# Performance work log

Hardware: AMD Instinct MI355X
Metric: run time of the kernel (lower is better)

The kernel has to match this reference:

```python
import jax, jax.numpy as jnp
import numpy as np

B, S, D = 2, 2048, 2048
NH, NKV, HD = 16, 4, 128
REP = NH // NKV
EPS = 1e-6
ROPE_THETA = 1e6


def setup_inputs() -> dict:
    key = jax.random.key(0)
    ks = jax.random.split(key, 6)
    x = jax.random.normal(ks[0], (B, S, D), jnp.float32)
    # real rotary embeddings: [S, HD]
    inv_freq = 1.0 / (ROPE_THETA ** (np.arange(0, HD, 2, dtype=np.float64) / HD))
    freqs = np.outer(np.arange(S, dtype=np.float64), inv_freq)
    emb = np.concatenate([freqs, freqs], axis=-1)
    cos = jnp.asarray(np.cos(emb), jnp.float32)
    sin = jnp.asarray(np.sin(emb), jnp.float32)
    scale = 1.0 / np.sqrt(D)
    Wq = jax.random.normal(ks[1], (D, NH * HD), jnp.float32) * scale   # [in, out]
    Wk = jax.random.normal(ks[2], (D, NKV * HD), jnp.float32) * scale
    Wv = jax.random.normal(ks[3], (D, NKV * HD), jnp.float32) * scale
    Wo = jax.random.normal(ks[4], (NH * HD, D), jnp.float32) * (1.0 / np.sqrt(NH * HD))
    q_norm_w = jnp.ones((HD,), jnp.float32)
    k_norm_w = jnp.ones((HD,), jnp.float32)
    return dict(x=x, cos=cos, sin=sin, Wq=Wq, Wk=Wk, Wv=Wv, Wo=Wo,
                q_norm_w=q_norm_w, k_norm_w=k_norm_w)


def _rms_norm(h, w):
    var = jnp.mean(h * h, axis=-1, keepdims=True)
    return w * (h * jax.lax.rsqrt(var + EPS))


def _rotate_half(h):
    h1, h2 = jnp.split(h, 2, axis=-1)
    return jnp.concatenate([-h2, h1], axis=-1)


def reference(x, cos, sin, Wq, Wk, Wv, Wo, q_norm_w, k_norm_w):
    b, s, _ = x.shape
    q = (x @ Wq).reshape(b, s, NH, HD)
    k = (x @ Wk).reshape(b, s, NKV, HD)
    v = (x @ Wv).reshape(b, s, NKV, HD)
    # per-head QK RMSNorm
    q = _rms_norm(q, q_norm_w)
    k = _rms_norm(k, k_norm_w)
    # RoPE: cos/sin [S,HD] -> broadcast over batch and heads
    c = cos[None, :, None, :]
    s_ = sin[None, :, None, :]
    q = q * c + _rotate_half(q) * s_
    k = k * c + _rotate_half(k) * s_
    # GQA: group q heads per kv head instead of materializing repeat_kv
    qg = q.reshape(b, s, NKV, REP, HD)
    scores = jnp.einsum('bqgrd,bkgd->bgrqk', qg, k) / np.sqrt(HD)
    causal = jnp.tril(jnp.ones((s, s), bool))  # [q,k]
    scores = jnp.where(causal, scores, -jnp.inf)
    probs = jax.nn.softmax(scores.astype(jnp.float32), axis=-1).astype(q.dtype)
    out = jnp.einsum('bgrqk,bkgd->bqgrd', probs, v).reshape(b, s, NH * HD)
    return out @ Wo
```

## Files before the change

### kernel.cpp

```cpp
#include <hip/hip_runtime.h>
#include <hip/hip_bf16.h>
#include <math.h>

#define B_ 2
#define S_ 2048
#define D_ 2048
#define NH_ 16
#define NKV_ 4
#define HD_ 128
#define EPS_ 1e-6f
#define SCALE_ 0.08838834764831845f
#define LOG2E_ 1.4426950408889634f
#define KOFF_ 2048
#define VOFF_ 2560
#define MINIT_ -1e30f

typedef float f32x4 __attribute__((ext_vector_type(4)));
typedef short bf16x8 __attribute__((ext_vector_type(8)));
typedef short short4v __attribute__((ext_vector_type(4)));
typedef float float4v __attribute__((ext_vector_type(4)));
typedef unsigned uint2v __attribute__((ext_vector_type(2)));
typedef unsigned uint4v __attribute__((ext_vector_type(4)));

static __device__ __forceinline__ short f2bf(float f) {
    union { float f; unsigned u; } x{f};
    unsigned r = (x.u + 0x7fff + ((x.u >> 16) & 1)) >> 16;
    return (short)r;
}
static __device__ __forceinline__ float bf2f(short s) {
    union { unsigned u; float f; } x; x.u = ((unsigned)(unsigned short)s) << 16; return x.f;
}
static __device__ __forceinline__ unsigned pack_bf2(float a, float b) {
    return __builtin_amdgcn_perm(__builtin_bit_cast(unsigned, b),
                                 __builtin_bit_cast(unsigned, a), 0x07060302u);
}

#define AS1(p) ((const __attribute__((address_space(1))) void*)(p))
#define AS3(p) ((__attribute__((address_space(3))) void*)(p))
static __device__ __forceinline__ void async16(const void* g, void* l) {
    __builtin_amdgcn_global_load_lds(AS1(g), AS3(l), 16, 0, 0);
}
#define SB_() __builtin_amdgcn_sched_barrier(0)

__global__ __launch_bounds__(256) void cast_kernel(const float* __restrict__ in,
                                                   short* __restrict__ out) {
    size_t i = ((size_t)blockIdx.x * 256 + threadIdx.x) * 4;
    float4v v = *(const float4v*)(in + i);
    short4v o; o.x = f2bf(v.x); o.y = f2bf(v.y); o.z = f2bf(v.z); o.w = f2bf(v.w);
    *(short4v*)(out + i) = o;
}

__global__ __launch_bounds__(256) void transpose_all_kernel(const float* __restrict__ Wq,
                                                            const float* __restrict__ Wk,
                                                            const float* __restrict__ Wv,
                                                            const float* __restrict__ Wo,
                                                            short* __restrict__ Wt,
                                                            short* __restrict__ Wot) {
    __shared__ float tile[64][65];
    const int bx = blockIdx.x, by = blockIdx.y;
    const float* src; short* dst; int N, nb;
    if (bx < 32)      { src = Wq; dst = Wt;                         N = 2048; nb = bx; }
    else if (bx < 40) { src = Wk; dst = Wt + (size_t)KOFF_ * 2048;  N = 512;  nb = bx - 32; }
    else if (bx < 48) { src = Wv; dst = Wt + (size_t)VOFF_ * 2048;  N = 512;  nb = bx - 40; }
    else              { src = Wo; dst = Wot;                        N = 2048; nb = bx - 48; }
    const int n0 = nb * 64, k0 = by * 64;
    const int tid = threadIdx.x;
    for (int r = 0; r < 16; ++r) {
        int k = r * 4 + (tid >> 6);
        int n = tid & 63;
        tile[k][n] = src[(size_t)(k0 + k) * N + n0 + n];
    }
    __syncthreads();
    for (int r = 0; r < 4; ++r) {
        int n  = r * 16 + (tid >> 4);
        int kk = (tid & 15) * 4;
        short4v o4;
        o4.x = f2bf(tile[kk + 0][n]); o4.y = f2bf(tile[kk + 1][n]);
        o4.z = f2bf(tile[kk + 2][n]); o4.w = f2bf(tile[kk + 3][n]);
        *(short4v*)&dst[(size_t)(n0 + n) * 2048 + k0 + kk] = o4;
    }
}

__global__ __launch_bounds__(512, 2) void gemm_oproj_kernel(const short* __restrict__ A,
                                                            const short* __restrict__ Bt,
                                                            float* __restrict__ C) {
    __shared__ __align__(16) short smem[49152];
    short* A0 = smem;
    short* A1 = smem + 8192;
    short* B0 = smem + 16384;
    short* B1 = smem + 32768;

    const int tid  = threadIdx.x;
    const int orig = blockIdx.y * 8 + blockIdx.x;
    const int swz  = (orig & 7) * 32 + (orig >> 3);
    const int bn = swz & 7, bm = swz >> 3;
    const int wave = tid >> 6, lane = tid & 63;
    const int quad = lane >> 4, l16 = lane & 15;
    const int wr = wave >> 2, wc = wave & 3;

    const short* Ag = A  + (size_t)(bm * 128) * 2048;
    const short* Bg = Bt + (size_t)(bn * 256) * 2048;

    f32x4 acc[4][4];
#pragma unroll
    for (int i = 0; i < 4; ++i)
#pragma unroll
        for (int j = 0; j < 4; ++j) acc[i][j] = (f32x4){0.f, 0.f, 0.f, 0.f};

    bf16x8 a[4][2], b0[2][2], b1[2][2];

    auto stage_half = [&](const short* gpanel, int t, int h, short* lslot) {
#pragma unroll
        for (int u = 0; u < 2; ++u) {
            int ci = u * 512 + tid;
            int r  = ci >> 3;
            int cb = ((ci & 7) * 16) ^ ((r & 7) << 4);
            async16(gpanel + (size_t)(h * 128 + r) * 2048 + t * 64 + (cb >> 1),
                    lslot + h * 8192 + ci * 8);
        }
    };

#define OLDA_(lbuf) \
    _Pragma("unroll") for (int mt = 0; mt < 4; ++mt) \
    _Pragma("unroll") for (int ks = 0; ks < 2; ++ks) { \
        int row_ = wr * 64 + mt * 16 + l16; \
        int cb_  = (ks * 64 + quad * 16) ^ ((row_ & 7) << 4); \
        a[mt][ks] = *(const bf16x8*)&(lbuf)[row_ * 64 + (cb_ >> 1)]; \
    }
#define OLDB_(lbuf, qn, breg) \
    _Pragma("unroll") for (int ntl = 0; ntl < 2; ++ntl) \
    _Pragma("unroll") for (int ks = 0; ks < 2; ++ks) { \
        int row_ = wc * 64 + (qn) * 32 + ntl * 16 + l16; \
        int cb_  = (ks * 64 + quad * 16) ^ ((row_ & 7) << 4); \
        breg[ntl][ks] = *(const bf16x8*)&(lbuf)[row_ * 64 + (cb_ >> 1)]; \
    }
#define OBAR_() __builtin_amdgcn_s_barrier()
#define OMFMA_(qn, breg) do { \
    __builtin_amdgcn_s_setprio(1); \
    _Pragma("unroll") for (int mt = 0; mt < 4; ++mt) \
    _Pragma("unroll") for (int ntl = 0; ntl < 2; ++ntl) \
    _Pragma("unroll") for (int ks = 0; ks < 2; ++ks) \
        acc[mt][(qn) * 2 + ntl] = __builtin_amdgcn_mfma_f32_16x16x32_bf16( \
            a[mt][ks], breg[ntl][ks], acc[mt][(qn) * 2 + ntl], 0, 0, 0); \
    __builtin_amdgcn_s_setprio(0); __builtin_amdgcn_s_barrier(); } while (0)

    stage_half(Bg, 0, 0, B0); stage_half(Bg, 0, 1, B0);
    stage_half(Ag, 0, 0, A0);
    asm volatile("s_waitcnt vmcnt(0)" ::: "memory");
    __builtin_amdgcn_s_barrier();

#pragma unroll 1
    for (int i = 0; i < 16; ++i) {
        const int tE = 2 * i, tO = 2 * i + 1;
        const bool more = (i < 15);

        stage_half(Ag, tO, 0, A1);
        stage_half(Bg, tO, 0, B1); stage_half(Bg, tO, 1, B1);
        OLDA_(A0); OLDB_(B0, 0, b0);
        OBAR_();
        OMFMA_(0, b0);

        if (more) {
            stage_half(Ag, tE + 2, 0, A0);
            asm volatile("s_waitcnt vmcnt(2)" ::: "memory");
        } else {
            asm volatile("s_waitcnt vmcnt(0)" ::: "memory");
        }
        OLDB_(B0, 1, b1);
        OBAR_();
        OMFMA_(1, b1);

        if (more) { stage_half(Bg, tE + 2, 0, B0); stage_half(Bg, tE + 2, 1, B0); }
        OLDA_(A1); OLDB_(B1, 0, b0);
        OBAR_();
        OMFMA_(0, b0);

        if (more) { asm volatile("s_waitcnt vmcnt(0)" ::: "memory"); }
        OLDB_(B1, 1, b1);
        OBAR_();
        OMFMA_(1, b1);
    }

#pragma unroll
    for (int mt = 0; mt < 4; ++mt)
#pragma unroll
        for (int nt = 0; nt < 4; ++nt)
#pragma unroll
            for (int j = 0; j < 4; ++j) {
                int row = bm * 128 + wr * 64 + mt * 16 + quad * 4 + j;
                int col = bn * 256 + wc * 64 + nt * 16 + l16;
                C[(size_t)row * 2048 + col] = acc[mt][nt][j];
            }
#undef OLDA_
#undef OLDB_
#undef OBAR_
#undef OMFMA_
}

#define QKV_ITERS 16

__global__ __launch_bounds__(512, 2) void qkv_fused_kernel(const short* __restrict__ xb,
                                                           const short* __restrict__ Wt,
                                                           const float* __restrict__ cosb,
                                                           const float* __restrict__ sinb,
                                                           const float* __restrict__ qw,
                                                           const float* __restrict__ kw,
                                                           short* __restrict__ q_rope,
                                                           short* __restrict__ k_rope,
                                                           short* __restrict__ vtr) {
    __shared__ __align__(16) short smem[65536];

    short* A0 = smem;
    short* A1 = smem + 8192;
    short* B0 = smem + 16384;
    short* B1 = smem + 40960;

    const int tid  = threadIdx.x;
    const int orig = blockIdx.y * 8 + blockIdx.x;
    const int swz  = (orig & 7) * 32 + (orig >> 3);
    const int bn = swz >> 5, bm = swz & 31;
    const int wave = tid >> 6, lane = tid & 63;
    const int quad = lane >> 4, l16 = lane & 15;
    const int wr = wave >> 2, wc = wave & 3;

    const short* Ag = xb + (size_t)(bm * 128) * 2048;
    const short* Bg = Wt + (size_t)(bn * 384) * 2048;

    f32x4 acc[4][6];
#pragma unroll
    for (int i = 0; i < 4; ++i)
#pragma unroll
        for (int j = 0; j < 6; ++j) acc[i][j] = (f32x4){0.f, 0.f, 0.f, 0.f};

    bf16x8 a[4][2], b0[3][2], b1[3][2];

    auto stage_half = [&](const short* gpanel, int t, int h, short* lslot) {
#pragma unroll
        for (int u = 0; u < 2; ++u) {
            int ci = u * 512 + tid;
            int r  = ci >> 3;
            int cb = ((ci & 7) * 16) ^ ((r & 7) << 4);
            async16(gpanel + (size_t)(h * 128 + r) * 2048 + t * 64 + (cb >> 1),
                    lslot + h * 8192 + ci * 8);
        }
    };

#define LDA_(lbuf) \
    _Pragma("unroll") for (int mt = 0; mt < 4; ++mt) \
    _Pragma("unroll") for (int ks = 0; ks < 2; ++ks) { \
        int row_ = wr * 64 + mt * 16 + l16; \
        int cb_  = (ks * 64 + quad * 16) ^ ((row_ & 7) << 4); \
        a[mt][ks] = *(const bf16x8*)&(lbuf)[row_ * 64 + (cb_ >> 1)]; \
    }
#define LDB_(lbuf, qn, breg) \
    _Pragma("unroll") for (int ntl = 0; ntl < 3; ++ntl) \
    _Pragma("unroll") for (int ks = 0; ks < 2; ++ks) { \
        int row_ = wc * 96 + (qn) * 48 + ntl * 16 + l16; \
        int cb_  = (ks * 64 + quad * 16) ^ ((row_ & 7) << 4); \
        breg[ntl][ks] = *(const bf16x8*)&(lbuf)[row_ * 64 + (cb_ >> 1)]; \
    }
#define PH_BAR() do { __builtin_amdgcn_sched_barrier(0); __builtin_amdgcn_s_barrier(); } while (0)
#define PH_MFMA24(qn, breg) do { \
        __builtin_amdgcn_s_setprio(1); \
        _Pragma("unroll") for (int mt = 0; mt < 4; ++mt) \
        _Pragma("unroll") for (int ntl = 0; ntl < 3; ++ntl) \
        _Pragma("unroll") for (int ks = 0; ks < 2; ++ks) \
            acc[mt][(qn) * 3 + ntl] = __builtin_amdgcn_mfma_f32_16x16x32_bf16( \
                a[mt][ks], breg[ntl][ks], acc[mt][(qn) * 3 + ntl], 0, 0, 0); \
        __builtin_amdgcn_s_setprio(0); \
        __builtin_amdgcn_sched_barrier(0); __builtin_amdgcn_s_barrier(); } while (0)

    stage_half(Bg, 0, 0, B0); stage_half(Bg, 0, 1, B0); stage_half(Bg, 0, 2, B0);
    stage_half(Ag, 0, 0, A0);
    stage_half(Ag, 1, 0, A1);
    asm volatile("s_waitcnt vmcnt(2)" ::: "memory");
    __builtin_amdgcn_s_barrier();

#pragma unroll 1
    for (int i = 0; i < QKV_ITERS; ++i) {
        const int tE = 2 * i, tO = 2 * i + 1;
        const bool more = (i < QKV_ITERS - 1);

        LDA_(A0); LDB_(B0, 0, b0);
        stage_half(Bg, tO, 0, B1); stage_half(Bg, tO, 1, B1); stage_half(Bg, tO, 2, B1);
        PH_BAR();
        PH_MFMA24(0, b0);

        LDB_(B0, 1, b1);
        if (more) {
            stage_half(Ag, tE + 2, 0, A0);
            asm volatile("s_waitcnt vmcnt(2)" ::: "memory");
        } else {
            asm volatile("s_waitcnt vmcnt(0)" ::: "memory");
        }
        PH_BAR();
        PH_MFMA24(1, b1);

        LDA_(A1); LDB_(B1, 0, b0);
        if (more) { stage_half(Bg, tE + 2, 0, B0); stage_half(Bg, tE + 2, 1, B0); stage_half(Bg, tE + 2, 2, B0); }
        PH_BAR();
        PH_MFMA24(0, b0);

        LDB_(B1, 1, b1);
        if (more) {
            stage_half(Ag, tO + 2, 0, A1);
            asm volatile("s_waitcnt vmcnt(2)" ::: "memory");
        }
        PH_BAR();
        PH_MFMA24(1, b1);
    }

#pragma unroll
    for (int mt = 0; mt < 4; ++mt) {
        int tok0 = bm * 128 + wr * 64 + mt * 16 + quad * 4;
        int bb = tok0 >> 11, s0 = tok0 & (S_ - 1);
#pragma unroll
        for (int nt = 0; nt < 6; ++nt) {
            int colh = wc * 96 + nt * 16;
            int gh = bn * 3 + (colh >> 7);
            if (gh >= 20) {
                int g = gh - 20;
                int d = (colh & 127) + l16;
                short4v o4;
                o4.x = f2bf(acc[mt][nt][0]); o4.y = f2bf(acc[mt][nt][1]);
                o4.z = f2bf(acc[mt][nt][2]); o4.w = f2bf(acc[mt][nt][3]);
                *(short4v*)&vtr[((size_t)(bb * NKV_ + g) * HD_ + d) * S_ + s0] = o4;
            }
        }
    }
    if (bn * 3 >= 20) return;

    short* ct = smem;
#pragma unroll
    for (int mt = 0; mt < 4; ++mt)
#pragma unroll
        for (int nt = 0; nt < 6; ++nt)
#pragma unroll
            for (int j = 0; j < 4; ++j)
                ct[(wr * 64 + mt * 16 + quad * 4 + j) * 386 + wc * 96 + nt * 16 + l16]
                    = f2bf(acc[mt][nt][j]);
    __syncthreads();

    if (tid < 384) {
        int hh = tid >> 7, row = tid & 127;
        int gh = bn * 3 + hh;
        if (gh < 20) {
            const bool isQ = gh < 16;
            const float osc = isQ ? (SCALE_ * LOG2E_) : 1.0f;
            const float* w = isQ ? qw : kw;
            const short* src = &ct[row * 386 + hh * 128];
            bf16x8 rv[16];
#pragma unroll
            for (int i = 0; i < 16; ++i) rv[i] = *(const bf16x8*)(src + i * 8);
            float ss = 0.f;
#pragma unroll
            for (int i = 0; i < 16; ++i)
#pragma unroll
                for (int j = 0; j < 8; ++j) { float f = bf2f(rv[i][j]); ss += f * f; }
            float rstd = rsqrtf(ss * (1.0f / HD_) + EPS_);
            int tok = bm * 128 + row;
            int bb = tok >> 11, s = tok & (S_ - 1);
            short* dst = isQ
                ? q_rope + ((size_t)(bb * S_ + s) * NH_ + gh) * HD_
                : k_rope + ((size_t)(bb * NKV_ + (gh - 16)) * S_ + s) * HD_;
#pragma unroll
            for (int sg = 0; sg < 16; ++sg) {
                int c0 = sg * 8, p0 = (sg ^ 8) * 8;
                bf16x8 ta = rv[sg], tb = rv[sg ^ 8];
                float sgn = (sg < 8) ? -1.0f : 1.0f;
                float4v cs0 = *(const float4v*)&cosb[(size_t)s * HD_ + c0];
                float4v cs1 = *(const float4v*)&cosb[(size_t)s * HD_ + c0 + 4];
                float4v sn0 = *(const float4v*)&sinb[(size_t)s * HD_ + c0];
                float4v sn1 = *(const float4v*)&sinb[(size_t)s * HD_ + c0 + 4];
                float ov[8];
#pragma unroll
                for (int i = 0; i < 8; ++i) {
                    float n1 = bf2f(ta[i]) * rstd * w[c0 + i];
                    float n2 = bf2f(tb[i]) * rstd * w[p0 + i];
                    float cs = (i < 4) ? cs0[i & 3] : cs1[i & 3];
                    float sn = (i < 4) ? sn0[i & 3] : sn1[i & 3];
                    ov[i] = (n1 * cs + sgn * n2 * sn) * osc;
                }
                uint4v wv;
#pragma unroll
                for (int i2 = 0; i2 < 4; ++i2)
                    wv[i2] = ((unsigned)(unsigned short)f2bf(ov[2 * i2])) |
                             ((unsigned)(unsigned short)f2bf(ov[2 * i2 + 1]) << 16);
                *(uint4v*)(dst + c0) = wv;
            }
        }
    }
#undef LDA_
#undef LDB_
#undef PH_BAR
#undef PH_MFMA24
}

__global__ __launch_bounds__(512, 1) void attn_kernel(const short* __restrict__ qr,
                                                      const short* __restrict__ kg,
                                                      const short* __restrict__ vt,
                                                      short* __restrict__ aout) {
    __shared__ __align__(16) short Ks[2][2][8192];
    __shared__ __align__(16) short Vs[2][2][8192];

    const int lin = blockIdx.x;
    const int b  = lin & 1;
    const int g  = (lin >> 1) & 3;
    const int hq = (lin >> 3) & 3;
    const int pr = lin >> 5;
    const int h  = g * 4 + hq;

    const int wave = threadIdx.x >> 6, lane = threadIdx.x & 63;
    const int quad = lane >> 4, l16 = lane & 15;
    const int half = wave >> 2;
    const int ww   = wave & 3;

    const short* kbase = kg + (size_t)(b * NKV_ + g) * S_ * HD_;
    const short* vbase = vt + (size_t)(b * NKV_ + g) * HD_ * S_;

    auto stage = [&](int kt, short* Kd, short* Vd) {
        const short* kt_base = kbase + (size_t)kt * 64 * HD_;
        const short* vt_base = vbase + kt * 64;
#pragma unroll
        for (int t = 0; t < 2; ++t) {
            int ci  = (wave * 2 + t) * 64 + lane;
            int key = ci >> 4;
            int c   = (ci & 15) ^ ((key ^ (key >> 2)) & 15);
            async16(kt_base + key * HD_ + c * 8, Kd + ci * 8);
        }
#pragma unroll
        for (int t = 0; t < 2; ++t) {
            int ci = (wave * 2 + t) * 64 + lane;
            int d  = ci >> 3;
            int c  = (ci & 7) ^ (d & 7);
            async16(vt_base + (size_t)d * S_ + c * 8, Vd + ci * 8);
        }
    };

#pragma unroll 1
    for (int ph = 0; ph < 2; ++ph) {
        const int qt    = ph ? (15 - pr) : pr;
        const int nhalf = qt + 1;
        const int qrow0 = qt * 128 + ww * 16 + l16;
        const int qrow1 = qrow0 + 64;

        bf16x8 qf[2][4];
#pragma unroll
        for (int qs = 0; qs < 2; ++qs) {
            const short* qp = qr + ((size_t)(b * S_ + (qs ? qrow1 : qrow0)) * NH_ + h) * HD_;
#pragma unroll
            for (int ks = 0; ks < 4; ++ks)
                qf[qs][ks] = *(const bf16x8*)(qp + ks * 32 + quad * 8);
        }

        f32x4 o[2][8];
#pragma unroll
        for (int qs = 0; qs < 2; ++qs)
#pragma unroll
            for (int i = 0; i < 8; ++i) o[qs][i] = (f32x4){0.f, 0.f, 0.f, 0.f};
        float m_i[2] = {MINIT_, MINIT_};
        float l_i[2] = {0.f, 0.f};

        stage(0, Ks[0][0], Vs[0][0]);
        stage(1, Ks[1][0], Vs[1][0]);
        int buf = 0;
#pragma unroll 1
        for (int i = 0; i < nhalf; ++i) {
            __syncthreads();
            if (i + 1 < nhalf) {
                stage(2 * i + 2, Ks[0][buf ^ 1], Vs[0][buf ^ 1]);
                stage(2 * i + 3, Ks[1][buf ^ 1], Vs[1][buf ^ 1]);
            }
            const short* Kb = Ks[half][buf];
            const short* Vb = Vs[half][buf];
            const int ktm = 2 * i + half;

            f32x4 acc[2][4];
#pragma unroll
            for (int qs = 0; qs < 2; ++qs)
#pragma unroll
                for (int t = 0; t < 4; ++t) acc[qs][t] = (f32x4){0.f, 0.f, 0.f, 0.f};
            __builtin_amdgcn_s_setprio(1);
#pragma unroll
            for (int t = 0; t < 4; ++t) {
                int lk = ((t >> 1) << 5) + ((l16 >> 2) << 3) + ((t & 1) << 2) + (l16 & 3);
                const short* kp = &Kb[lk * 128];
                int pm = (lk ^ (lk >> 2)) & 15;
#pragma unroll
                for (int ks = 0; ks < 4; ++ks) {
                    bf16x8 kf = *(const bf16x8*)(kp + (((ks * 4 + quad) ^ pm) * 8));
                    acc[0][t] = __builtin_amdgcn_mfma_f32_16x16x32_bf16(kf, qf[0][ks], acc[0][t], 0, 0, 0);
                    acc[1][t] = __builtin_amdgcn_mfma_f32_16x16x32_bf16(kf, qf[1][ks], acc[1][t], 0, 0, 0);
                }
            }
            __builtin_amdgcn_s_setprio(0);
            const int key_base = ktm * 64;
#pragma unroll
            for (int qs = 0; qs < 2; ++qs) {
                int qmin = qt * 128 + qs * 64 + ww * 16;
                int qrow = qs ? qrow1 : qrow0;
                if (key_base + 63 > qmin) {
#pragma unroll
                    for (int t = 0; t < 4; ++t)
#pragma unroll
                        for (int j = 0; j < 4; ++j) {
                            int kl = key_base + ((t >> 1) << 5) + (quad << 3) + ((t & 1) << 2) + j;
                            if (kl > qrow) acc[qs][t][j] = -INFINITY;
                        }
                }
            }
            unsigned pk[2][2][4];
#pragma unroll
            for (int qs = 0; qs < 2; ++qs) {
                float mx = m_i[qs];
#pragma unroll
                for (int t = 0; t < 4; ++t)
#pragma unroll
                    for (int j = 0; j < 4; ++j) mx = fmaxf(mx, acc[qs][t][j]);
                mx = fmaxf(mx, __shfl_xor(mx, 16));
                mx = fmaxf(mx, __shfl_xor(mx, 32));
                float al = __builtin_amdgcn_exp2f(m_i[qs] - mx);
                m_i[qs] = mx;
                float rs = 0.f;
                float p[4][4];
#pragma unroll
                for (int t = 0; t < 4; ++t)
#pragma unroll
                    for (int j = 0; j < 4; ++j) {
                        float e = __builtin_amdgcn_exp2f(acc[qs][t][j] - mx);
                        p[t][j] = e;
                        rs += e;
                    }
                rs += __shfl_xor(rs, 16);
                rs += __shfl_xor(rs, 32);
                l_i[qs] = al * l_i[qs] + rs;
#pragma unroll
                for (int d8 = 0; d8 < 8; ++d8)
#pragma unroll
                    for (int j = 0; j < 4; ++j) o[qs][d8][j] *= al;
#pragma unroll
                for (int grp = 0; grp < 2; ++grp) {
                    pk[qs][grp][0] = pack_bf2(p[2 * grp][0],     p[2 * grp][1]);
                    pk[qs][grp][1] = pack_bf2(p[2 * grp][2],     p[2 * grp][3]);
                    pk[qs][grp][2] = pack_bf2(p[2 * grp + 1][0], p[2 * grp + 1][1]);
                    pk[qs][grp][3] = pack_bf2(p[2 * grp + 1][2], p[2 * grp + 1][3]);
                }
            }
            __builtin_amdgcn_s_setprio(1);
#pragma unroll
            for (int grp = 0; grp < 2; ++grp) {
                union { unsigned u[4]; bf16x8 v; } pb0, pb1;
#pragma unroll
                for (int i2 = 0; i2 < 4; ++i2) { pb0.u[i2] = pk[0][grp][i2]; pb1.u[i2] = pk[1][grp][i2]; }
#pragma unroll
                for (int d8 = 0; d8 < 8; ++d8) {
                    int d = d8 * 16 + l16;
                    bf16x8 vf = *(const bf16x8*)&Vb[d * 64 + (((grp * 4 + quad) ^ (d & 7)) * 8)];
                    o[0][d8] = __builtin_amdgcn_mfma_f32_16x16x32_bf16(vf, pb0.v, o[0][d8], 0, 0, 0);
                    o[1][d8] = __builtin_amdgcn_mfma_f32_16x16x32_bf16(vf, pb1.v, o[1][d8], 0, 0, 0);
                }
            }
            __builtin_amdgcn_s_setprio(0);
            buf ^= 1;
        }

        __syncthreads();
        float* exch = (float*)(ww < 2 ? &Ks[0][0][0] : &Vs[0][0][0]);
        float* slot = exch + ((size_t)((ww & 1) * 64 + lane) * 68);
        if (half == 1) {
#pragma unroll
            for (int qs = 0; qs < 2; ++qs) {
#pragma unroll
                for (int d8 = 0; d8 < 8; ++d8)
#pragma unroll
                    for (int j = 0; j < 4; ++j)
                        slot[qs * 32 + d8 * 4 + j] = o[qs][d8][j];
                slot[64 + qs] = m_i[qs];
                slot[66 + qs] = l_i[qs];
            }
        }
        __syncthreads();
        if (half == 0) {
#pragma unroll
            for (int qs = 0; qs < 2; ++qs) {
                float mB = slot[64 + qs], lB = slot[66 + qs];
                float m  = fmaxf(m_i[qs], mB);
                float wA = __builtin_amdgcn_exp2f(m_i[qs] - m);
                float wB = __builtin_amdgcn_exp2f(mB - m);
                float il = 1.0f / (l_i[qs] * wA + lB * wB);
                int qrow = qs ? qrow1 : qrow0;
                short* op = aout + ((size_t)(b * S_ + qrow) * NH_ + h) * HD_ + quad * 4;
#pragma unroll
                for (int d8 = 0; d8 < 8; ++d8) {
                    float v0 = (o[qs][d8][0] * wA + slot[qs * 32 + d8 * 4 + 0] * wB) * il;
                    float v1 = (o[qs][d8][1] * wA + slot[qs * 32 + d8 * 4 + 1] * wB) * il;
                    float v2 = (o[qs][d8][2] * wA + slot[qs * 32 + d8 * 4 + 2] * wB) * il;
                    float v3 = (o[qs][d8][3] * wA + slot[qs * 32 + d8 * 4 + 3] * wB) * il;
                    uint2v wv;
                    wv.x = ((unsigned)(unsigned short)f2bf(v0)) |
                           ((unsigned)(unsigned short)f2bf(v1) << 16);
                    wv.y = ((unsigned)(unsigned short)f2bf(v2)) |
                           ((unsigned)(unsigned short)f2bf(v3) << 16);
                    *(uint2v*)(op + d8 * 16) = wv;
                }
            }
        }
        __syncthreads();
    }
}

extern "C" void kernel_launch(void* const* d_in, const int* in_sizes, int n_in,
                              void* d_out, int out_size, void* d_ws, size_t ws_size,
                              hipStream_t stream) {
    (void)in_sizes; (void)n_in; (void)out_size; (void)ws_size;
    const float* x    = (const float*)d_in[0];
    const float* cosb = (const float*)d_in[1];
    const float* sinb = (const float*)d_in[2];
    const float* Wq   = (const float*)d_in[3];
    const float* Wk   = (const float*)d_in[4];
    const float* Wv   = (const float*)d_in[5];
    const float* Wo   = (const float*)d_in[6];
    const float* qw   = (const float*)d_in[7];
    const float* kw   = (const float*)d_in[8];
    float* out = (float*)d_out;

    char* ws = (char*)d_ws;
    short* xb     = (short*)ws;  ws += (size_t)4096 * 2048 * 2;
    short* Wt     = (short*)ws;  ws += (size_t)3072 * 2048 * 2;
    short* Wot    = (short*)ws;  ws += (size_t)2048 * 2048 * 2;
    short* q_rope = (short*)ws;  ws += (size_t)4096 * 2048 * 2;
    short* k_rope = (short*)ws;  ws += (size_t)4096 * 512 * 2;
    short* vt     = (short*)ws;  ws += (size_t)4096 * 512 * 2;
    short* a_out  = (short*)ws;  ws += (size_t)4096 * 2048 * 2;

    const int M = B_ * S_;

    cast_kernel<<<M * 2048 / 1024, 256, 0, stream>>>(x, xb);
    transpose_all_kernel<<<dim3(80, 32), 256, 0, stream>>>(Wq, Wk, Wv, Wo, Wt, Wot);

    qkv_fused_kernel<<<dim3(8, 32), 512, 0, stream>>>(
        xb, Wt, cosb, sinb, qw, kw, q_rope, k_rope, vt);

    attn_kernel<<<256, 512, 0, stream>>>(q_rope, k_rope, vt, a_out);

    gemm_oproj_kernel<<<dim3(8, 32), 512, 0, stream>>>(a_out, Wot, out);
}
```

Before: 289.7 us.

## Parallelize QK-norm/RoPE epilogue across all threads with shuffle-reduced row sums

The QKV GEMM epilogue now computes per-row sum-of-squares directly from fp32 accumulators using 16-lane xor shuffles and stores the partial sums in shared memory. The RMSNorm+RoPE pass is redistributed so all 512 threads each handle one 8-element segment per iteration, instead of 384 threads each processing a full 128-wide head row. This is meant to cut per-thread serial work and register pressure and to spread the global stores across more threads. The norm is now taken from fp32 values rather than bf16-rounded ones, and the shared tile stride changes from 386 to 384, which may alter bank-conflict behaviour. The partial sums also need additional shared memory.

```diff
diff --git a/kernel.cpp b/kernel.cpp
--- a/kernel.cpp
+++ b/kernel.cpp
@@ -331,64 +331,85 @@
     if (bn * 3 >= 20) return;
 
     short* ct = smem;
+    float* ps = (float*)(smem + 49152);
+    {
+#pragma unroll
+        for (int nt = 0; nt < 6; ++nt) {
+            float s[4][4];
+#pragma unroll
+            for (int mt = 0; mt < 4; ++mt)
+#pragma unroll
+                for (int j = 0; j < 4; ++j)
+                    s[mt][j] = acc[mt][nt][j] * acc[mt][nt][j];
+#pragma unroll
+            for (int off = 1; off < 16; off <<= 1)
+#pragma unroll
+                for (int mt = 0; mt < 4; ++mt)
+#pragma unroll
+                    for (int j = 0; j < 4; ++j)
+                        s[mt][j] += __shfl_xor(s[mt][j], off);
+            if (l16 == 0) {
+#pragma unroll
+                for (int mt = 0; mt < 4; ++mt)
+#pragma unroll
+                    for (int j = 0; j < 4; ++j)
+                        ps[(wc * 6 + nt) * 128 + wr * 64 + mt * 16 + quad * 4 + j] = s[mt][j];
+            }
+        }
+    }
 #pragma unroll
     for (int mt = 0; mt < 4; ++mt)
 #pragma unroll
         for (int nt = 0; nt < 6; ++nt)
 #pragma unroll
             for (int j = 0; j < 4; ++j)
-                ct[(wr * 64 + mt * 16 + quad * 4 + j) * 386 + wc * 96 + nt * 16 + l16]
+                ct[(wr * 64 + mt * 16 + quad * 4 + j) * 384 + wc * 96 + nt * 16 + l16]
                     = f2bf(acc[mt][nt][j]);
     __syncthreads();
 
-    if (tid < 384) {
-        int hh = tid >> 7, row = tid & 127;
-        int gh = bn * 3 + hh;
-        if (gh < 20) {
-            const bool isQ = gh < 16;
-            const float osc = isQ ? (SCALE_ * LOG2E_) : 1.0f;
-            const float* w = isQ ? qw : kw;
-            const short* src = &ct[row * 386 + hh * 128];
-            bf16x8 rv[16];
-#pragma unroll
-            for (int i = 0; i < 16; ++i) rv[i] = *(const bf16x8*)(src + i * 8);
-            float ss = 0.f;
-#pragma unroll
-            for (int i = 0; i < 16; ++i)
-#pragma unroll
-                for (int j = 0; j < 8; ++j) { float f = bf2f(rv[i][j]); ss += f * f; }
-            float rstd = rsqrtf(ss * (1.0f / HD_) + EPS_);
-            int tok = bm * 128 + row;
-            int bb = tok >> 11, s = tok & (S_ - 1);
-            short* dst = isQ
-                ? q_rope + ((size_t)(bb * S_ + s) * NH_ + gh) * HD_
-                : k_rope + ((size_t)(bb * NKV_ + (gh - 16)) * S_ + s) * HD_;
-#pragma unroll
-            for (int sg = 0; sg < 16; ++sg) {
-                int c0 = sg * 8, p0 = (sg ^ 8) * 8;
-                bf16x8 ta = rv[sg], tb = rv[sg ^ 8];
-                float sgn = (sg < 8) ? -1.0f : 1.0f;
-                float4v cs0 = *(const float4v*)&cosb[(size_t)s * HD_ + c0];
-                float4v cs1 = *(const float4v*)&cosb[(size_t)s * HD_ + c0 + 4];
-                float4v sn0 = *(const float4v*)&sinb[(size_t)s * HD_ + c0];
-                float4v sn1 = *(const float4v*)&sinb[(size_t)s * HD_ + c0 + 4];
-                float ov[8];
-#pragma unroll
-                for (int i = 0; i < 8; ++i) {
-                    float n1 = bf2f(ta[i]) * rstd * w[c0 + i];
-                    float n2 = bf2f(tb[i]) * rstd * w[p0 + i];
-                    float cs = (i < 4) ? cs0[i & 3] : cs1[i & 3];
-                    float sn = (i < 4) ? sn0[i & 3] : sn1[i & 3];
-                    ov[i] = (n1 * cs + sgn * n2 * sn) * osc;
-                }
-                uint4v wv;
-#pragma unroll
-                for (int i2 = 0; i2 < 4; ++i2)
-                    wv[i2] = ((unsigned)(unsigned short)f2bf(ov[2 * i2])) |
-                             ((unsigned)(unsigned short)f2bf(ov[2 * i2 + 1]) << 16);
-                *(uint4v*)(dst + c0) = wv;
-            }
-        }
+#pragma unroll 1
+    for (int it = 0; it < 12; ++it) {
+        int f = it * 512 + tid;
+        int seg = f & 15;
+        int rh  = f >> 4;
+        int row = rh & 127, head = rh >> 7;
+        int gh = bn * 3 + head;
+        if (gh >= 20) continue;
+        const bool isQ = gh < 16;
+        const float osc = isQ ? (SCALE_ * LOG2E_) : 1.0f;
+        const float* w = isQ ? qw : kw;
+        float ss = 0.f;
+#pragma unroll
+        for (int c = 0; c < 8; ++c) ss += ps[(head * 8 + c) * 128 + row];
+        float rstd = rsqrtf(ss * (1.0f / HD_) + EPS_);
+        int tok = bm * 128 + row;
+        int bb = tok >> 11, s = tok & (S_ - 1);
+        int c0 = seg * 8, p0 = (seg ^ 8) * 8;
+        bf16x8 ta = *(const bf16x8*)&ct[row * 384 + head * 128 + c0];
+        bf16x8 tb = *(const bf16x8*)&ct[row * 384 + head * 128 + p0];
+        float sgn = (seg < 8) ? -1.0f : 1.0f;
+        float4v cs0 = *(const float4v*)&cosb[(size_t)s * HD_ + c0];
+        float4v cs1 = *(const float4v*)&cosb[(size_t)s * HD_ + c0 + 4];
+        float4v sn0 = *(const float4v*)&sinb[(size_t)s * HD_ + c0];
+        float4v sn1 = *(const float4v*)&sinb[(size_t)s * HD_ + c0 + 4];
+        float ov[8];
+#pragma unroll
+        for (int i = 0; i < 8; ++i) {
+            float n1 = bf2f(ta[i]) * rstd * w[c0 + i];
+            float n2 = bf2f(tb[i]) * rstd * w[p0 + i];
+            float cs = (i < 4) ? cs0[i & 3] : cs1[i & 3];
+            float sn = (i < 4) ? sn0[i & 3] : sn1[i & 3];
+            ov[i] = (n1 * cs + sgn * n2 * sn) * osc;
+        }
+        uint4v wv;
+#pragma unroll
+        for (int i2 = 0; i2 < 4; ++i2)
+            wv[i2] = ((unsigned)(unsigned short)f2bf(ov[2 * i2])) |
+                     ((unsigned)(unsigned short)f2bf(ov[2 * i2 + 1]) << 16);
+        short* dst = isQ
+            ? q_rope + ((size_t)(bb * S_ + s) * NH_ + gh) * HD_ + c0
+            : k_rope + ((size_t)(bb * NKV_ + (gh - 16)) * S_ + s) * HD_ + c0;
+        *(uint4v*)dst = wv;
     }
 #undef LDA_
 #undef LDB_
```

Measured after the change: 279.1 us. 1.04x faster.
